# Performance work log

Hardware: AMD Instinct MI355X
Metric: run time of the kernel (lower is better)

The kernel has to match this reference:

```python
import jax, jax.numpy as jnp
import numpy as np

K = 9          # self.k
DILATION = 1   # self.dilation
L_B = 90       # banded window width (hardcoded in source)


def setup_inputs() -> dict:
    key = jax.random.key(0)
    x = jax.random.normal(key, (4, 64, 8192, 1), dtype=jnp.float32)
    return {"x": x}


def reference(x):
    # F.normalize(x, p=2, dim=1): L2-normalize over the feature (dims) axis
    eps = 1e-12
    norm = jnp.sqrt(jnp.sum(x * x, axis=1, keepdims=True))
    x = x / jnp.maximum(norm, eps)

    # (B, D, N, 1) -> (B, N, D)
    xt = jnp.squeeze(x, -1).transpose(0, 2, 1)
    B, N, D = xt.shape
    kk = K * DILATION  # top-k width used inside dense_knn_matrix

    # pairwise squared distances: |xi|^2 - 2 xi.xj + |xj|^2  -> (B, N, N)
    sq = jnp.sum(xt * xt, axis=-1, keepdims=True)
    dist = sq - 2.0 * jnp.einsum('bnd,bmd->bnm', xt, xt) + sq.transpose(0, 2, 1)

    # band mask: allowed columns j satisfy i - (L_B - 1) <= j <= i
    # (mask_u kills strict upper triangle; mask_d kills cols below the band)
    i = jnp.arange(N)
    allowed = (i[None, :] <= i[:, None]) & (i[None, :] >= i[:, None] - (L_B - 1))
    fmax = jnp.finfo(dist.dtype).max
    dist = jnp.where(allowed[None], dist, fmax)

    # k nearest = top-k of negative distance
    _, nn_idx = jax.lax.top_k(-dist, kk)  # (B, N, kk) int32

    # diagonal neighbor propagation: for row j < L_B, cols > j get row j's
    # nearest-neighbor index (vectorized form of the source's python loop)
    temp = nn_idx[:, :L_B, 0:1]                      # (B, L_B, 1)
    rows = jnp.arange(L_B)[None, :, None]
    cols = jnp.arange(kk)[None, None, :]
    head = jnp.where(cols > rows, temp, nn_idx[:, :L_B])
    nn_idx = jnp.concatenate([head, nn_idx[:, L_B:]], axis=1)

    center = jnp.broadcast_to(i[None, :, None], (B, N, kk)).astype(nn_idx.dtype)
    edge = jnp.stack([nn_idx, center], axis=0)       # (2, B, N, kk)

    # DenseDilated: stride-slice last axis by dilation, then overwrite the
    # first L_B rows with the undilated first K neighbors
    e = edge[:, :, :, ::DILATION]                    # (2, B, N, K)
    e = e.at[:, :, :L_B].set(edge[:, :, :L_B, :K])
    return e
```

## Files before the change

### kernel.cpp

```cpp
#include <hip/hip_runtime.h>
#include <hip/hip_bf16.h>
#include <stdint.h>

#define NPTS 8192
#define DIM  64
#define NB   4
#define KK   9
#define BQ   64
#define RROWS 160
#define SD2  72
#define UD   65

typedef short bf16x8 __attribute__((ext_vector_type(8)));
typedef float f32x4  __attribute__((ext_vector_type(4)));

__global__ __launch_bounds__(512, 4) void knn_fused(const float* __restrict__ x,
                                                    int* __restrict__ out) {
    __shared__ uint32_t ud[RROWS * UD];
    __shared__ ushort   sb[RROWS * SD2];
    __shared__ float    rnArr[RROWS];

    float* psumA = (float*)ud;
    float* psumB = (float*)ud + 512;

    const int tid = threadIdx.x;
    const int blk = blockIdx.x;
    const int L   = (blk & 7) * 64 + (blk >> 3);
    const int b   = L >> 7;
    const int n0  = (L & 127) << 6;
    const int gbase = n0 - 89;

    const float* xb = x + (size_t)b * DIM * NPTS;

    {
        const int g  = tid & 127;
        const int dh = (tid >> 7) << 4;
        const int gg = gbase + g;
        const bool ok = (gg >= 0 && gg < NPTS);
        const float* src = xb + (ok ? gg : 0);
        float s = 0.f;
#pragma unroll
        for (int j = 0; j < 2; ++j) {
            uint32_t pk[4];
#pragma unroll
            for (int e = 0; e < 4; ++e) {
                int d = dh + j * 8 + e * 2;
                float v0 = ok ? src[(size_t)d * NPTS] : 0.f;
                float v1 = ok ? src[(size_t)(d + 1) * NPTS] : 0.f;
                s += v0 * v0 + v1 * v1;
                __hip_bfloat162 h2 = __float22bfloat162_rn(make_float2(v0, v1));
                pk[e] = *reinterpret_cast<uint32_t*>(&h2);
            }
            *reinterpret_cast<uint4*>(&sb[(size_t)g * SD2 + dh + j * 8]) =
                make_uint4(pk[0], pk[1], pk[2], pk[3]);
        }
        psumA[tid] = s;
    }
    {
        const int g  = 128 + (tid & 31);
        const int c  = tid >> 5;
        const int gg = gbase + g;
        const bool ok = (gg >= 0 && gg < NPTS);
        const float* src = xb + (ok ? gg : 0);
        float s = 0.f;
        uint32_t pk[2];
#pragma unroll
        for (int e = 0; e < 2; ++e) {
            int d = c * 4 + e * 2;
            float v0 = ok ? src[(size_t)d * NPTS] : 0.f;
            float v1 = ok ? src[(size_t)(d + 1) * NPTS] : 0.f;
            s += v0 * v0 + v1 * v1;
            __hip_bfloat162 h2 = __float22bfloat162_rn(make_float2(v0, v1));
            pk[e] = *reinterpret_cast<uint32_t*>(&h2);
        }
        *reinterpret_cast<uint2*>(&sb[(size_t)g * SD2 + c * 4]) = make_uint2(pk[0], pk[1]);
        psumB[tid] = s;
    }
    __syncthreads();

    const int w  = tid >> 6;
    const int l  = tid & 63;
    const int qt = w >> 1;
    const int h  = w & 1;
    const int lr = l & 15;
    const int lk = l >> 4;
    const int nrt = 4 - h;

    const ushort* ap = &sb[(size_t)(89 + qt * 16 + lr) * SD2 + lk * 8];
    bf16x8 a0 = *reinterpret_cast<const bf16x8*>(ap);
    bf16x8 a1 = *reinterpret_cast<const bf16x8*>(ap + 32);
    bf16x8 bfr[4][2];
#pragma unroll
    for (int i = 0; i < 4; ++i) {
        if (i < nrt) {
            const int rto = h * 4 + i;
            const ushort* bp = &sb[(size_t)(qt * 16 + rto * 16 + lr) * SD2 + lk * 8];
            bfr[i][0] = *reinterpret_cast<const bf16x8*>(bp);
            bfr[i][1] = *reinterpret_cast<const bf16x8*>(bp + 32);
        }
    }

    if (tid < 128) {
        float s = psumA[tid] + psumA[tid + 128] + psumA[tid + 256] + psumA[tid + 384];
        rnArr[tid] = 1.0f / fmaxf(sqrtf(s), 1e-12f);
    } else if (tid < 160) {
        int rr = tid - 128;
        float s = 0.f;
#pragma unroll
        for (int k = 0; k < 16; ++k) s += psumB[rr + 32 * k];
        rnArr[tid] = 1.0f / fmaxf(sqrtf(s), 1e-12f);
    }
    __syncthreads();

    {
        float rq[4];
#pragma unroll
        for (int j = 0; j < 4; ++j) rq[j] = rnArr[89 + qt * 16 + lk * 4 + j];
        const int q0 = qt * 16 + lk * 4;
#pragma unroll
        for (int i = 0; i < 4; ++i) {
            if (i < nrt) {
                f32x4 acc = {0.f, 0.f, 0.f, 0.f};
                acc = __builtin_amdgcn_mfma_f32_16x16x32_bf16(a0, bfr[i][0], acc, 0, 0, 0);
                acc = __builtin_amdgcn_mfma_f32_16x16x32_bf16(a1, bfr[i][1], acc, 0, 0, 0);
                const int rto = h * 4 + i;
                const int r = qt * 16 + rto * 16 + lr;
                const float rnr = rnArr[r];
#pragma unroll
                for (int j = 0; j < 4; ++j) {
                    float p = acc[j] * rq[j] * rnr;
                    float dist = 2.0f - 2.0f * p;
                    uint32_t uu = __float_as_uint(dist);
                    uu = (uu & 0x80000000u) ? ~uu : (uu | 0x80000000u);
                    int rel = r - (q0 + j);
                    ud[r * UD + q0 + j] = (uu & 0xFFFFFF80u) | ((uint32_t)rel & 127u);
                }
            }
        }
    }
    __syncthreads();

    {
        const int ql = l >> 3;
        const int s  = l & 7;
        const int q  = (w << 3) | ql;
        const int n  = n0 + q;

        uint32_t key[12];
#pragma unroll
        for (int t = 0; t < 12; ++t) {
            int wofs = s + 8 * t;
            int m = n - 89 + wofs;
            bool ok = (wofs <= 89) && (m >= 0);
            int r = q + (ok ? wofs : 0);
            uint32_t raw = ud[r * UD + q];
            key[t] = ok ? raw : 0xFFFFFFFFu;
        }

        uint32_t prev = 0;
        int omKeep = n;
        int om8 = n;
#pragma unroll
        for (int j = 0; j < KK; ++j) {
            uint32_t mn = 0xFFFFFFFFu;
#pragma unroll
            for (int t = 0; t < 12; ++t) {
                uint32_t cand = (key[t] > prev) ? key[t] : 0xFFFFFFFFu;
                mn = (cand < mn) ? cand : mn;
            }
            uint32_t o;
            o = (uint32_t)__shfl_xor((int)mn, 1); mn = (o < mn) ? o : mn;
            o = (uint32_t)__shfl_xor((int)mn, 2); mn = (o < mn) ? o : mn;
            o = (uint32_t)__shfl_xor((int)mn, 4); mn = (o < mn) ? o : mn;
            int om = (mn == 0xFFFFFFFFu) ? n : (n - 89 + (int)(mn & 127u));
            if (j < 8) {
                if (s == j) omKeep = om;
            } else {
                om8 = om;
            }
            prev = mn;
        }

        const int base0 = (b * NPTS + n) * KK;
        const int base1 = NB * NPTS * KK + base0;
        out[base0 + s] = omKeep;
        out[base1 + s] = n;
        if (s == 0) {
            out[base0 + 8] = om8;
            out[base1 + 8] = n;
        }
    }
}

extern "C" void kernel_launch(void* const* d_in, const int* in_sizes, int n_in,
                              void* d_out, int out_size, void* d_ws, size_t ws_size,
                              hipStream_t stream) {
    const float* x = (const float*)d_in[0];
    int* out = (int*)d_out;
    knn_fused<<<NB * (NPTS / BQ), 512, 0, stream>>>(x, out);
}
```

Before: 13.41 us.

## Split into bf16 prep kernel and core kNN kernel via workspace

Adds a prep kernel that converts x to row-major bf16 and precomputes inverse norms into the workspace. The core kernel then loads the 160-row halo with coalesced 16-byte loads instead of strided fp32 gathers, which removes the redundant per-block conversion of overlapping halo rows. It also shrinks the distance buffer to a query-major banded layout with only in-band writes. The cost is a second kernel launch and a global-memory round trip, and the old fused kernel is kept as a fallback when no workspace is provided.

```diff
diff --git a/kernel.cpp b/kernel.cpp
--- a/kernel.cpp
+++ b/kernel.cpp
@@ -9,19 +9,65 @@
 #define BQ   64
 #define RROWS 160
 #define SD2  72
-#define UD   65
+#define UD2  91
+#define WS_NEED (NB * NPTS * DIM * 2 + NB * NPTS * 4)
 
 typedef short bf16x8 __attribute__((ext_vector_type(8)));
 typedef float f32x4  __attribute__((ext_vector_type(4)));
 
-__global__ __launch_bounds__(512, 4) void knn_fused(const float* __restrict__ x,
-                                                    int* __restrict__ out) {
-    __shared__ uint32_t ud[RROWS * UD];
+__global__ __launch_bounds__(256, 4) void prep(const float* __restrict__ x,
+                                               ushort* __restrict__ y,
+                                               float* __restrict__ rnG) {
+    __shared__ uint32_t st[64 * 36];
+    __shared__ float psum[256];
+
+    const int tid = threadIdx.x;
+    const int blk = blockIdx.x;
+    const int b   = blk >> 7;
+    const int n0  = (blk & 127) << 6;
+    const int nl  = tid & 63;
+    const int dh  = (tid >> 6) << 4;
+
+    const float* src = x + (size_t)b * DIM * NPTS + n0 + nl;
+    float s = 0.f;
+#pragma unroll
+    for (int j = 0; j < 2; ++j) {
+        uint32_t pk[4];
+#pragma unroll
+        for (int e = 0; e < 4; ++e) {
+            int d = dh + j * 8 + e * 2;
+            float v0 = src[(size_t)d * NPTS];
+            float v1 = src[(size_t)(d + 1) * NPTS];
+            s += v0 * v0 + v1 * v1;
+            __hip_bfloat162 h2 = __float22bfloat162_rn(make_float2(v0, v1));
+            pk[e] = *reinterpret_cast<uint32_t*>(&h2);
+        }
+        *reinterpret_cast<uint4*>(&st[nl * 36 + dh / 2 + j * 4]) =
+            make_uint4(pk[0], pk[1], pk[2], pk[3]);
+    }
+    psum[tid] = s;
+    __syncthreads();
+
+    if (tid < 64) {
+        float ss = psum[tid] + psum[tid + 64] + psum[tid + 128] + psum[tid + 192];
+        rnG[(size_t)b * NPTS + n0 + tid] = 1.0f / fmaxf(sqrtf(ss), 1e-12f);
+    }
+
+    uint4* yv = (uint4*)(y + ((size_t)b * NPTS + n0) * DIM);
+#pragma unroll
+    for (int i = 0; i < 2; ++i) {
+        int c = tid + 256 * i;
+        int row = c >> 3, col = c & 7;
+        yv[c] = *reinterpret_cast<const uint4*>(&st[row * 36 + col * 4]);
+    }
+}
+
+__global__ __launch_bounds__(512, 4) void knn_core(const ushort* __restrict__ y,
+                                                   const float* __restrict__ rnG,
+                                                   int* __restrict__ out) {
     __shared__ ushort   sb[RROWS * SD2];
+    __shared__ uint32_t ud[BQ * UD2];
     __shared__ float    rnArr[RROWS];
-
-    float* psumA = (float*)ud;
-    float* psumB = (float*)ud + 512;
 
     const int tid = threadIdx.x;
     const int blk = blockIdx.x;
@@ -30,51 +76,24 @@
     const int n0  = (L & 127) << 6;
     const int gbase = n0 - 89;
 
-    const float* xb = x + (size_t)b * DIM * NPTS;
-
-    {
-        const int g  = tid & 127;
-        const int dh = (tid >> 7) << 4;
-        const int gg = gbase + g;
-        const bool ok = (gg >= 0 && gg < NPTS);
-        const float* src = xb + (ok ? gg : 0);
-        float s = 0.f;
-#pragma unroll
-        for (int j = 0; j < 2; ++j) {
-            uint32_t pk[4];
-#pragma unroll
-            for (int e = 0; e < 4; ++e) {
-                int d = dh + j * 8 + e * 2;
-                float v0 = ok ? src[(size_t)d * NPTS] : 0.f;
-                float v1 = ok ? src[(size_t)(d + 1) * NPTS] : 0.f;
-                s += v0 * v0 + v1 * v1;
-                __hip_bfloat162 h2 = __float22bfloat162_rn(make_float2(v0, v1));
-                pk[e] = *reinterpret_cast<uint32_t*>(&h2);
-            }
-            *reinterpret_cast<uint4*>(&sb[(size_t)g * SD2 + dh + j * 8]) =
-                make_uint4(pk[0], pk[1], pk[2], pk[3]);
-        }
-        psumA[tid] = s;
-    }
-    {
-        const int g  = 128 + (tid & 31);
-        const int c  = tid >> 5;
-        const int gg = gbase + g;
-        const bool ok = (gg >= 0 && gg < NPTS);
-        const float* src = xb + (ok ? gg : 0);
-        float s = 0.f;
-        uint32_t pk[2];
-#pragma unroll
-        for (int e = 0; e < 2; ++e) {
-            int d = c * 4 + e * 2;
-            float v0 = ok ? src[(size_t)d * NPTS] : 0.f;
-            float v1 = ok ? src[(size_t)(d + 1) * NPTS] : 0.f;
-            s += v0 * v0 + v1 * v1;
-            __hip_bfloat162 h2 = __float22bfloat162_rn(make_float2(v0, v1));
-            pk[e] = *reinterpret_cast<uint32_t*>(&h2);
-        }
-        *reinterpret_cast<uint2*>(&sb[(size_t)g * SD2 + c * 4]) = make_uint2(pk[0], pk[1]);
-        psumB[tid] = s;
+    const ushort* yb = y + (size_t)b * NPTS * DIM;
+
+#pragma unroll
+    for (int i = 0; i < 3; ++i) {
+        int c = tid + 512 * i;
+        if (c < RROWS * 8) {
+            int row = c >> 3, col = c & 7;
+            int m = gbase + row;
+            bool ok = (m >= 0 && m < NPTS);
+            const uint4* src =
+                reinterpret_cast<const uint4*>(yb + (size_t)(ok ? m : 0) * DIM) + col;
+            uint4 v = ok ? *src : make_uint4(0u, 0u, 0u, 0u);
+            *reinterpret_cast<uint4*>(&sb[row * SD2 + col * 8]) = v;
+        }
+    }
+    if (tid < RROWS) {
+        int m = gbase + tid;
+        rnArr[tid] = (m >= 0 && m < NPTS) ? rnG[(size_t)b * NPTS + m] : 1.0f;
     }
     __syncthreads();
 
@@ -89,51 +108,34 @@
     const ushort* ap = &sb[(size_t)(89 + qt * 16 + lr) * SD2 + lk * 8];
     bf16x8 a0 = *reinterpret_cast<const bf16x8*>(ap);
     bf16x8 a1 = *reinterpret_cast<const bf16x8*>(ap + 32);
-    bf16x8 bfr[4][2];
+
+    float rq[4];
+#pragma unroll
+    for (int j = 0; j < 4; ++j) rq[j] = rnArr[89 + qt * 16 + lk * 4 + j];
+    const int q0 = qt * 16 + lk * 4;
+
 #pragma unroll
     for (int i = 0; i < 4; ++i) {
         if (i < nrt) {
             const int rto = h * 4 + i;
-            const ushort* bp = &sb[(size_t)(qt * 16 + rto * 16 + lr) * SD2 + lk * 8];
-            bfr[i][0] = *reinterpret_cast<const bf16x8*>(bp);
-            bfr[i][1] = *reinterpret_cast<const bf16x8*>(bp + 32);
-        }
-    }
-
-    if (tid < 128) {
-        float s = psumA[tid] + psumA[tid + 128] + psumA[tid + 256] + psumA[tid + 384];
-        rnArr[tid] = 1.0f / fmaxf(sqrtf(s), 1e-12f);
-    } else if (tid < 160) {
-        int rr = tid - 128;
-        float s = 0.f;
-#pragma unroll
-        for (int k = 0; k < 16; ++k) s += psumB[rr + 32 * k];
-        rnArr[tid] = 1.0f / fmaxf(sqrtf(s), 1e-12f);
-    }
-    __syncthreads();
-
-    {
-        float rq[4];
-#pragma unroll
-        for (int j = 0; j < 4; ++j) rq[j] = rnArr[89 + qt * 16 + lk * 4 + j];
-        const int q0 = qt * 16 + lk * 4;
-#pragma unroll
-        for (int i = 0; i < 4; ++i) {
-            if (i < nrt) {
-                f32x4 acc = {0.f, 0.f, 0.f, 0.f};
-                acc = __builtin_amdgcn_mfma_f32_16x16x32_bf16(a0, bfr[i][0], acc, 0, 0, 0);
-                acc = __builtin_amdgcn_mfma_f32_16x16x32_bf16(a1, bfr[i][1], acc, 0, 0, 0);
-                const int rto = h * 4 + i;
-                const int r = qt * 16 + rto * 16 + lr;
-                const float rnr = rnArr[r];
-#pragma unroll
-                for (int j = 0; j < 4; ++j) {
+            const int rbase = qt * 16 + rto * 16;
+            const ushort* bp = &sb[(size_t)(rbase + lr) * SD2 + lk * 8];
+            bf16x8 b0 = *reinterpret_cast<const bf16x8*>(bp);
+            bf16x8 b1 = *reinterpret_cast<const bf16x8*>(bp + 32);
+            f32x4 acc = {0.f, 0.f, 0.f, 0.f};
+            acc = __builtin_amdgcn_mfma_f32_16x16x32_bf16(a0, b0, acc, 0, 0, 0);
+            acc = __builtin_amdgcn_mfma_f32_16x16x32_bf16(a1, b1, acc, 0, 0, 0);
+            const int r = rbase + lr;
+            const float rnr = rnArr[r];
+#pragma unroll
+            for (int j = 0; j < 4; ++j) {
+                int rel = r - (q0 + j);
+                if (rel >= 0 && rel <= 89) {
                     float p = acc[j] * rq[j] * rnr;
                     float dist = 2.0f - 2.0f * p;
                     uint32_t uu = __float_as_uint(dist);
                     uu = (uu & 0x80000000u) ? ~uu : (uu | 0x80000000u);
-                    int rel = r - (q0 + j);
-                    ud[r * UD + q0 + j] = (uu & 0xFFFFFF80u) | ((uint32_t)rel & 127u);
+                    ud[(q0 + j) * UD2 + rel] = (uu & 0xFFFFFF80u) | (uint32_t)rel;
                 }
             }
         }
@@ -152,8 +154,7 @@
             int wofs = s + 8 * t;
             int m = n - 89 + wofs;
             bool ok = (wofs <= 89) && (m >= 0);
-            int r = q + (ok ? wofs : 0);
-            uint32_t raw = ud[r * UD + q];
+            uint32_t raw = ud[q * UD2 + (ok ? wofs : 0)];
             key[t] = ok ? raw : 0xFFFFFFFFu;
         }
 
@@ -192,10 +193,196 @@
     }
 }
 
+#define UDF 65
+__global__ __launch_bounds__(512, 4) void knn_fused(const float* __restrict__ x,
+                                                    int* __restrict__ out) {
+    __shared__ uint32_t ud[RROWS * UDF];
+    __shared__ ushort   sb[RROWS * SD2];
+    __shared__ float    rnArr[RROWS];
+
+    float* psumA = (float*)ud;
+    float* psumB = (float*)ud + 512;
+
+    const int tid = threadIdx.x;
+    const int blk = blockIdx.x;
+    const int L   = (blk & 7) * 64 + (blk >> 3);
+    const int b   = L >> 7;
+    const int n0  = (L & 127) << 6;
+    const int gbase = n0 - 89;
+
+    const float* xb = x + (size_t)b * DIM * NPTS;
+
+    {
+        const int g  = tid & 127;
+        const int dh = (tid >> 7) << 4;
+        const int gg = gbase + g;
+        const bool ok = (gg >= 0 && gg < NPTS);
+        const float* src = xb + (ok ? gg : 0);
+        float s = 0.f;
+#pragma unroll
+        for (int j = 0; j < 2; ++j) {
+            uint32_t pk[4];
+#pragma unroll
+            for (int e = 0; e < 4; ++e) {
+                int d = dh + j * 8 + e * 2;
+                float v0 = ok ? src[(size_t)d * NPTS] : 0.f;
+                float v1 = ok ? src[(size_t)(d + 1) * NPTS] : 0.f;
+                s += v0 * v0 + v1 * v1;
+                __hip_bfloat162 h2 = __float22bfloat162_rn(make_float2(v0, v1));
+                pk[e] = *reinterpret_cast<uint32_t*>(&h2);
+            }
+            *reinterpret_cast<uint4*>(&sb[(size_t)g * SD2 + dh + j * 8]) =
+                make_uint4(pk[0], pk[1], pk[2], pk[3]);
+        }
+        psumA[tid] = s;
+    }
+    {
+        const int g  = 128 + (tid & 31);
+        const int c  = tid >> 5;
+        const int gg = gbase + g;
+        const bool ok = (gg >= 0 && gg < NPTS);
+        const float* src = xb + (ok ? gg : 0);
+        float s = 0.f;
+        uint32_t pk[2];
+#pragma unroll
+        for (int e = 0; e < 2; ++e) {
+            int d = c * 4 + e * 2;
+            float v0 = ok ? src[(size_t)d * NPTS] : 0.f;
+            float v1 = ok ? src[(size_t)(d + 1) * NPTS] : 0.f;
+            s += v0 * v0 + v1 * v1;
+            __hip_bfloat162 h2 = __float22bfloat162_rn(make_float2(v0, v1));
+            pk[e] = *reinterpret_cast<uint32_t*>(&h2);
+        }
+        *reinterpret_cast<uint2*>(&sb[(size_t)g * SD2 + c * 4]) = make_uint2(pk[0], pk[1]);
+        psumB[tid] = s;
+    }
+    __syncthreads();
+
+    const int w  = tid >> 6;
+    const int l  = tid & 63;
+    const int qt = w >> 1;
+    const int h  = w & 1;
+    const int lr = l & 15;
+    const int lk = l >> 4;
+    const int nrt = 4 - h;
+
+    const ushort* ap = &sb[(size_t)(89 + qt * 16 + lr) * SD2 + lk * 8];
+    bf16x8 a0 = *reinterpret_cast<const bf16x8*>(ap);
+    bf16x8 a1 = *reinterpret_cast<const bf16x8*>(ap + 32);
+    bf16x8 bfr[4][2];
+#pragma unroll
+    for (int i = 0; i < 4; ++i) {
+        if (i < nrt) {
+            const int rto = h * 4 + i;
+            const ushort* bp = &sb[(size_t)(qt * 16 + rto * 16 + lr) * SD2 + lk * 8];
+            bfr[i][0] = *reinterpret_cast<const bf16x8*>(bp);
+            bfr[i][1] = *reinterpret_cast<const bf16x8*>(bp + 32);
+        }
+    }
+
+    if (tid < 128) {
+        float s = psumA[tid] + psumA[tid + 128] + psumA[tid + 256] + psumA[tid + 384];
+        rnArr[tid] = 1.0f / fmaxf(sqrtf(s), 1e-12f);
+    } else if (tid < 160) {
+        int rr = tid - 128;
+        float s = 0.f;
+#pragma unroll
+        for (int k = 0; k < 16; ++k) s += psumB[rr + 32 * k];
+        rnArr[tid] = 1.0f / fmaxf(sqrtf(s), 1e-12f);
+    }
+    __syncthreads();
+
+    {
+        float rq[4];
+#pragma unroll
+        for (int j = 0; j < 4; ++j) rq[j] = rnArr[89 + qt * 16 + lk * 4 + j];
+        const int q0 = qt * 16 + lk * 4;
+#pragma unroll
+        for (int i = 0; i < 4; ++i) {
+            if (i < nrt) {
+                f32x4 acc = {0.f, 0.f, 0.f, 0.f};
+                acc = __builtin_amdgcn_mfma_f32_16x16x32_bf16(a0, bfr[i][0], acc, 0, 0, 0);
+                acc = __builtin_amdgcn_mfma_f32_16x16x32_bf16(a1, bfr[i][1], acc, 0, 0, 0);
+                const int rto = h * 4 + i;
+                const int r = qt * 16 + rto * 16 + lr;
+                const float rnr = rnArr[r];
+#pragma unroll
+                for (int j = 0; j < 4; ++j) {
+                    float p = acc[j] * rq[j] * rnr;
+                    float dist = 2.0f - 2.0f * p;
+                    uint32_t uu = __float_as_uint(dist);
+                    uu = (uu & 0x80000000u) ? ~uu : (uu | 0x80000000u);
+                    int rel = r - (q0 + j);
+                    ud[r * UDF + q0 + j] = (uu & 0xFFFFFF80u) | ((uint32_t)rel & 127u);
+                }
+            }
+        }
+    }
+    __syncthreads();
+
+    {
+        const int ql = l >> 3;
+        const int s  = l & 7;
+        const int q  = (w << 3) | ql;
+        const int n  = n0 + q;
+
+        uint32_t key[12];
+#pragma unroll
+        for (int t = 0; t < 12; ++t) {
+            int wofs = s + 8 * t;
+            int m = n - 89 + wofs;
+            bool ok = (wofs <= 89) && (m >= 0);
+            int r = q + (ok ? wofs : 0);
+            uint32_t raw = ud[r * UDF + q];
+            key[t] = ok ? raw : 0xFFFFFFFFu;
+        }
+
+        uint32_t prev = 0;
+        int omKeep = n;
+        int om8 = n;
+#pragma unroll
+        for (int j = 0; j < KK; ++j) {
+            uint32_t mn = 0xFFFFFFFFu;
+#pragma unroll
+            for (int t = 0; t < 12; ++t) {
+                uint32_t cand = (key[t] > prev) ? key[t] : 0xFFFFFFFFu;
+                mn = (cand < mn) ? cand : mn;
+            }
+            uint32_t o;
+            o = (uint32_t)__shfl_xor((int)mn, 1); mn = (o < mn) ? o : mn;
+            o = (uint32_t)__shfl_xor((int)mn, 2); mn = (o < mn) ? o : mn;
+            o = (uint32_t)__shfl_xor((int)mn, 4); mn = (o < mn) ? o : mn;
+            int om = (mn == 0xFFFFFFFFu) ? n : (n - 89 + (int)(mn & 127u));
+            if (j < 8) {
+                if (s == j) omKeep = om;
+            } else {
+                om8 = om;
+            }
+            prev = mn;
+        }
+
+        const int base0 = (b * NPTS + n) * KK;
+        const int base1 = NB * NPTS * KK + base0;
+        out[base0 + s] = omKeep;
+        out[base1 + s] = n;
+        if (s == 0) {
+            out[base0 + 8] = om8;
+            out[base1 + 8] = n;
+        }
+    }
+}
+
 extern "C" void kernel_launch(void* const* d_in, const int* in_sizes, int n_in,
                               void* d_out, int out_size, void* d_ws, size_t ws_size,
                               hipStream_t stream) {
     const float* x = (const float*)d_in[0];
     int* out = (int*)d_out;
-    knn_fused<<<NB * (NPTS / BQ), 512, 0, stream>>>(x, out);
+    if (d_ws != nullptr && ws_size >= (size_t)WS_NEED) {
+        ushort* y   = (ushort*)d_ws;
+        float*  rnG = (float*)((char*)d_ws + (size_t)NB * NPTS * DIM * 2);
+        prep<<<NB * (NPTS / 64), 256, 0, stream>>>(x, y, rnG);
+        knn_core<<<NB * (NPTS / BQ), 512, 0, stream>>>(y, rnG, out);
+    } else {
+        knn_fused<<<NB * (NPTS / BQ), 512, 0, stream>>>(x, out);
+    }
 }
```

Measured after the change: 18.46 us. 1.38x slower.

## Reduce row norms with wave shuffles and compact distance buffer to band layout

Applied to the files above, without the earlier changes.

Row squared-norm partial sums are now reduced with xor-shuffles inside groups of lanes, which removes the shared-memory partial-sum arrays and one block-wide barrier. The distance scratch buffer is re-laid out per query as a band of 91 entries, storing only in-band pairs, which shrinks shared memory and may allow more resident blocks. B fragments are now loaded inside the MFMA loop instead of being preloaded, and the load thread mapping changes to four lanes per point, which alters global access coalescing.

```diff
diff --git a/kernel.cpp b/kernel.cpp
--- a/kernel.cpp
+++ b/kernel.cpp
@@ -9,19 +9,16 @@
 #define BQ   64
 #define RROWS 160
 #define SD2  72
-#define UD   65
+#define UD2  91
 
 typedef short bf16x8 __attribute__((ext_vector_type(8)));
 typedef float f32x4  __attribute__((ext_vector_type(4)));
 
 __global__ __launch_bounds__(512, 4) void knn_fused(const float* __restrict__ x,
                                                     int* __restrict__ out) {
-    __shared__ uint32_t ud[RROWS * UD];
     __shared__ ushort   sb[RROWS * SD2];
+    __shared__ uint32_t ud[BQ * UD2];
     __shared__ float    rnArr[RROWS];
-
-    float* psumA = (float*)ud;
-    float* psumB = (float*)ud + 512;
 
     const int tid = threadIdx.x;
     const int blk = blockIdx.x;
@@ -33,10 +30,10 @@
     const float* xb = x + (size_t)b * DIM * NPTS;
 
     {
-        const int g  = tid & 127;
-        const int dh = (tid >> 7) << 4;
-        const int gg = gbase + g;
-        const bool ok = (gg >= 0 && gg < NPTS);
+        const int g    = tid >> 2;
+        const int part = tid & 3;
+        const int gg   = gbase + g;
+        const bool ok  = (gg >= 0 && gg < NPTS);
         const float* src = xb + (ok ? gg : 0);
         float s = 0.f;
 #pragma unroll
@@ -44,37 +41,43 @@
             uint32_t pk[4];
 #pragma unroll
             for (int e = 0; e < 4; ++e) {
-                int d = dh + j * 8 + e * 2;
+                int d = part * 16 + j * 8 + e * 2;
                 float v0 = ok ? src[(size_t)d * NPTS] : 0.f;
                 float v1 = ok ? src[(size_t)(d + 1) * NPTS] : 0.f;
                 s += v0 * v0 + v1 * v1;
                 __hip_bfloat162 h2 = __float22bfloat162_rn(make_float2(v0, v1));
                 pk[e] = *reinterpret_cast<uint32_t*>(&h2);
             }
-            *reinterpret_cast<uint4*>(&sb[(size_t)g * SD2 + dh + j * 8]) =
+            *reinterpret_cast<uint4*>(&sb[(size_t)g * SD2 + part * 16 + j * 8]) =
                 make_uint4(pk[0], pk[1], pk[2], pk[3]);
         }
-        psumA[tid] = s;
+        s += __shfl_xor(s, 1);
+        s += __shfl_xor(s, 2);
+        if (part == 0) rnArr[g] = 1.0f / fmaxf(sqrtf(s), 1e-12f);
     }
     {
-        const int g  = 128 + (tid & 31);
-        const int c  = tid >> 5;
-        const int gg = gbase + g;
+        const int g   = 128 + (tid >> 4);
+        const int p16 = tid & 15;
+        const int gg  = gbase + g;
         const bool ok = (gg >= 0 && gg < NPTS);
         const float* src = xb + (ok ? gg : 0);
         float s = 0.f;
         uint32_t pk[2];
 #pragma unroll
         for (int e = 0; e < 2; ++e) {
-            int d = c * 4 + e * 2;
+            int d = p16 * 4 + e * 2;
             float v0 = ok ? src[(size_t)d * NPTS] : 0.f;
             float v1 = ok ? src[(size_t)(d + 1) * NPTS] : 0.f;
             s += v0 * v0 + v1 * v1;
             __hip_bfloat162 h2 = __float22bfloat162_rn(make_float2(v0, v1));
             pk[e] = *reinterpret_cast<uint32_t*>(&h2);
         }
-        *reinterpret_cast<uint2*>(&sb[(size_t)g * SD2 + c * 4]) = make_uint2(pk[0], pk[1]);
-        psumB[tid] = s;
+        *reinterpret_cast<uint2*>(&sb[(size_t)g * SD2 + p16 * 4]) = make_uint2(pk[0], pk[1]);
+        s += __shfl_xor(s, 1);
+        s += __shfl_xor(s, 2);
+        s += __shfl_xor(s, 4);
+        s += __shfl_xor(s, 8);
+        if (p16 == 0) rnArr[g] = 1.0f / fmaxf(sqrtf(s), 1e-12f);
     }
     __syncthreads();
 
@@ -89,51 +92,34 @@
     const ushort* ap = &sb[(size_t)(89 + qt * 16 + lr) * SD2 + lk * 8];
     bf16x8 a0 = *reinterpret_cast<const bf16x8*>(ap);
     bf16x8 a1 = *reinterpret_cast<const bf16x8*>(ap + 32);
-    bf16x8 bfr[4][2];
+
+    float rq[4];
+#pragma unroll
+    for (int j = 0; j < 4; ++j) rq[j] = rnArr[89 + qt * 16 + lk * 4 + j];
+    const int q0 = qt * 16 + lk * 4;
+
 #pragma unroll
     for (int i = 0; i < 4; ++i) {
         if (i < nrt) {
             const int rto = h * 4 + i;
-            const ushort* bp = &sb[(size_t)(qt * 16 + rto * 16 + lr) * SD2 + lk * 8];
-            bfr[i][0] = *reinterpret_cast<const bf16x8*>(bp);
-            bfr[i][1] = *reinterpret_cast<const bf16x8*>(bp + 32);
-        }
-    }
-
-    if (tid < 128) {
-        float s = psumA[tid] + psumA[tid + 128] + psumA[tid + 256] + psumA[tid + 384];
-        rnArr[tid] = 1.0f / fmaxf(sqrtf(s), 1e-12f);
-    } else if (tid < 160) {
-        int rr = tid - 128;
-        float s = 0.f;
+            const int rbase = qt * 16 + rto * 16;
+            const ushort* bp = &sb[(size_t)(rbase + lr) * SD2 + lk * 8];
+            bf16x8 b0 = *reinterpret_cast<const bf16x8*>(bp);
+            bf16x8 b1 = *reinterpret_cast<const bf16x8*>(bp + 32);
+            f32x4 acc = {0.f, 0.f, 0.f, 0.f};
+            acc = __builtin_amdgcn_mfma_f32_16x16x32_bf16(a0, b0, acc, 0, 0, 0);
+            acc = __builtin_amdgcn_mfma_f32_16x16x32_bf16(a1, b1, acc, 0, 0, 0);
+            const int r = rbase + lr;
+            const float rnr = rnArr[r];
 #pragma unroll
-        for (int k = 0; k < 16; ++k) s += psumB[rr + 32 * k];
-        rnArr[tid] = 1.0f / fmaxf(sqrtf(s), 1e-12f);
-    }
-    __syncthreads();
-
-    {
-        float rq[4];
-#pragma unroll
-        for (int j = 0; j < 4; ++j) rq[j] = rnArr[89 + qt * 16 + lk * 4 + j];
-        const int q0 = qt * 16 + lk * 4;
-#pragma unroll
-        for (int i = 0; i < 4; ++i) {
-            if (i < nrt) {
-                f32x4 acc = {0.f, 0.f, 0.f, 0.f};
-                acc = __builtin_amdgcn_mfma_f32_16x16x32_bf16(a0, bfr[i][0], acc, 0, 0, 0);
-                acc = __builtin_amdgcn_mfma_f32_16x16x32_bf16(a1, bfr[i][1], acc, 0, 0, 0);
-                const int rto = h * 4 + i;
-                const int r = qt * 16 + rto * 16 + lr;
-                const float rnr = rnArr[r];
-#pragma unroll
-                for (int j = 0; j < 4; ++j) {
+            for (int j = 0; j < 4; ++j) {
+                int rel = r - (q0 + j);
+                if (rel >= 0 && rel <= 89) {
                     float p = acc[j] * rq[j] * rnr;
                     float dist = 2.0f - 2.0f * p;
                     uint32_t uu = __float_as_uint(dist);
                     uu = (uu & 0x80000000u) ? ~uu : (uu | 0x80000000u);
-                    int rel = r - (q0 + j);
-                    ud[r * UD + q0 + j] = (uu & 0xFFFFFF80u) | ((uint32_t)rel & 127u);
+                    ud[(q0 + j) * UD2 + rel] = (uu & 0xFFFFFF80u) | (uint32_t)rel;
                 }
             }
         }
@@ -152,8 +138,7 @@
             int wofs = s + 8 * t;
             int m = n - 89 + wofs;
             bool ok = (wofs <= 89) && (m >= 0);
-            int r = q + (ok ? wofs : 0);
-            uint32_t raw = ud[r * UD + q];
+            uint32_t raw = ud[q * UD2 + (ok ? wofs : 0)];
             key[t] = ok ? raw : 0xFFFFFFFFu;
         }
 
```

Result: slower. 15.62 us (+16.4%).

## Make each wave own its queries' distance keys and drop block barrier

Applied to the files above, without the earlier changes.

Both waves of a pair now compute all seven row tiles for their 16-query strip. Each wave writes only the 8 queries it later runs top-k on, so the `__syncthreads` between the distance stage and the selection stage can be removed. The distance buffer becomes query-major and holds only the 90 in-band entries per query, which shrinks LDS use and gives the top-k reads a different bank pattern. The cost is duplicated MFMA work and per-tile B-fragment loads from LDS instead of preloading them into registers.

```diff
diff --git a/kernel.cpp b/kernel.cpp
--- a/kernel.cpp
+++ b/kernel.cpp
@@ -9,14 +9,14 @@
 #define BQ   64
 #define RROWS 160
 #define SD2  72
-#define UD   65
+#define UD2  91
 
 typedef short bf16x8 __attribute__((ext_vector_type(8)));
 typedef float f32x4  __attribute__((ext_vector_type(4)));
 
 __global__ __launch_bounds__(512, 4) void knn_fused(const float* __restrict__ x,
                                                     int* __restrict__ out) {
-    __shared__ uint32_t ud[RROWS * UD];
+    __shared__ uint32_t ud[BQ * UD2];
     __shared__ ushort   sb[RROWS * SD2];
     __shared__ float    rnArr[RROWS];
 
@@ -81,24 +81,13 @@
     const int w  = tid >> 6;
     const int l  = tid & 63;
     const int qt = w >> 1;
-    const int h  = w & 1;
     const int lr = l & 15;
     const int lk = l >> 4;
-    const int nrt = 4 - h;
+    const bool packHalf = ((lk >> 1) == (w & 1));
 
     const ushort* ap = &sb[(size_t)(89 + qt * 16 + lr) * SD2 + lk * 8];
     bf16x8 a0 = *reinterpret_cast<const bf16x8*>(ap);
     bf16x8 a1 = *reinterpret_cast<const bf16x8*>(ap + 32);
-    bf16x8 bfr[4][2];
-#pragma unroll
-    for (int i = 0; i < 4; ++i) {
-        if (i < nrt) {
-            const int rto = h * 4 + i;
-            const ushort* bp = &sb[(size_t)(qt * 16 + rto * 16 + lr) * SD2 + lk * 8];
-            bfr[i][0] = *reinterpret_cast<const bf16x8*>(bp);
-            bfr[i][1] = *reinterpret_cast<const bf16x8*>(bp + 32);
-        }
-    }
 
     if (tid < 128) {
         float s = psumA[tid] + psumA[tid + 128] + psumA[tid + 256] + psumA[tid + 384];
@@ -118,27 +107,31 @@
         for (int j = 0; j < 4; ++j) rq[j] = rnArr[89 + qt * 16 + lk * 4 + j];
         const int q0 = qt * 16 + lk * 4;
 #pragma unroll
-        for (int i = 0; i < 4; ++i) {
-            if (i < nrt) {
-                f32x4 acc = {0.f, 0.f, 0.f, 0.f};
-                acc = __builtin_amdgcn_mfma_f32_16x16x32_bf16(a0, bfr[i][0], acc, 0, 0, 0);
-                acc = __builtin_amdgcn_mfma_f32_16x16x32_bf16(a1, bfr[i][1], acc, 0, 0, 0);
-                const int rto = h * 4 + i;
-                const int r = qt * 16 + rto * 16 + lr;
-                const float rnr = rnArr[r];
+        for (int rto = 0; rto < 7; ++rto) {
+            const int rbase = qt * 16 + rto * 16;
+            const ushort* bp = &sb[(size_t)(rbase + lr) * SD2 + lk * 8];
+            bf16x8 b0 = *reinterpret_cast<const bf16x8*>(bp);
+            bf16x8 b1 = *reinterpret_cast<const bf16x8*>(bp + 32);
+            f32x4 acc = {0.f, 0.f, 0.f, 0.f};
+            acc = __builtin_amdgcn_mfma_f32_16x16x32_bf16(a0, b0, acc, 0, 0, 0);
+            acc = __builtin_amdgcn_mfma_f32_16x16x32_bf16(a1, b1, acc, 0, 0, 0);
+            const int r = rbase + lr;
+            const float rnr = rnArr[r];
+            if (packHalf) {
 #pragma unroll
                 for (int j = 0; j < 4; ++j) {
-                    float p = acc[j] * rq[j] * rnr;
-                    float dist = 2.0f - 2.0f * p;
-                    uint32_t uu = __float_as_uint(dist);
-                    uu = (uu & 0x80000000u) ? ~uu : (uu | 0x80000000u);
                     int rel = r - (q0 + j);
-                    ud[r * UD + q0 + j] = (uu & 0xFFFFFF80u) | ((uint32_t)rel & 127u);
+                    if (rel >= 0 && rel <= 89) {
+                        float p = acc[j] * rq[j] * rnr;
+                        float dist = 2.0f - 2.0f * p;
+                        uint32_t uu = __float_as_uint(dist);
+                        uu = (uu & 0x80000000u) ? ~uu : (uu | 0x80000000u);
+                        ud[(q0 + j) * UD2 + rel] = (uu & 0xFFFFFF80u) | (uint32_t)rel;
+                    }
                 }
             }
         }
     }
-    __syncthreads();
 
     {
         const int ql = l >> 3;
@@ -152,8 +145,7 @@
             int wofs = s + 8 * t;
             int m = n - 89 + wofs;
             bool ok = (wofs <= 89) && (m >= 0);
-            int r = q + (ok ? wofs : 0);
-            uint32_t raw = ud[r * UD + q];
+            uint32_t raw = ud[q * UD2 + (ok ? wofs : 0)];
             key[t] = ok ? raw : 0xFFFFFFFFu;
         }
 
```

New measurement: 14.75 us. +10.0%, slower.
